# Optimization experiments

Measured on AMD Instinct MI355X. Metric: run time of the kernel, lower is better.

The kernel has to match this reference:

```python
import jax, jax.numpy as jnp
import numpy as np

# LinearAdderV1: out[b,o] = sum_i (input[b,i] + weight[o,i]); out *= bias[o]
# The broadcast-add-then-reduce is mathematically separable:
#   sum_i (x[b,i] + w[o,i]) = sum_i x[b,i] + sum_i w[o,i]
# so we compute it without materializing the (B, O, I) intermediate. Same math,
# identical up to fp summation order.

B = 4096
IN = 4096
OUT = 4096


def setup_inputs() -> dict:
    key = jax.random.key(0)
    k1, k2, k3 = jax.random.split(key, 3)
    inp = jax.random.normal(k1, (B, IN), dtype=jnp.float32)
    # kaiming_uniform-ish scale for weight, uniform bias in [-1/sqrt(fan_in), +)
    bound_w = float(np.sqrt(6.0 / ((1.0 + 5.0) * IN)))  # a=sqrt(5) => gain^2=2/(1+5)
    weight = jax.random.uniform(k2, (OUT, IN), dtype=jnp.float32, minval=-bound_w, maxval=bound_w)
    bound_b = float(1.0 / np.sqrt(IN))
    bias_param = jax.random.uniform(k3, (OUT,), dtype=jnp.float32, minval=-bound_b, maxval=bound_b)
    return {"input": inp, "weight": weight, "bias_param": bias_param}


def reference(input, weight, bias_param):
    # (B, 1) + (1, OUT) -> (B, OUT)
    x_sum = jnp.sum(input, axis=-1, keepdims=True)          # (B, 1)
    w_sum = jnp.sum(weight, axis=-1)                        # (OUT,)
    out = x_sum + w_sum[None, :]                            # (B, OUT)
    out = out * bias_param[None, :]
    return out
```

## Files before the change

kernel.cpp:

```cpp
#include <hip/hip_runtime.h>

#define B_DIM   4096
#define IN_DIM  4096
#define OUT_DIM 4096

typedef float floatx4 __attribute__((ext_vector_type(4)));

__global__ __launch_bounds__(256) void rowsum_kernel(
    const float* __restrict__ input, const float* __restrict__ weight,
    const float* __restrict__ bias, float* __restrict__ ws)
{
    const int wave = threadIdx.x >> 6;
    const int lane = threadIdx.x & 63;
    const int row  = blockIdx.x * 4 + wave;

    const float* src = (row < B_DIM)
        ? input  + (size_t)row * IN_DIM
        : weight + (size_t)(row - B_DIM) * IN_DIM;
    const float4* src4 = (const float4*)src;

    float4 v[16];
    #pragma unroll
    for (int k = 0; k < 16; ++k)
        v[k] = src4[lane + k * 64];

    float s0 = 0.f, s1 = 0.f, s2 = 0.f, s3 = 0.f;
    #pragma unroll
    for (int k = 0; k < 16; k += 4) {
        s0 += (v[k+0].x + v[k+0].y) + (v[k+0].z + v[k+0].w);
        s1 += (v[k+1].x + v[k+1].y) + (v[k+1].z + v[k+1].w);
        s2 += (v[k+2].x + v[k+2].y) + (v[k+2].z + v[k+2].w);
        s3 += (v[k+3].x + v[k+3].y) + (v[k+3].z + v[k+3].w);
    }
    float s = (s0 + s1) + (s2 + s3);

    #pragma unroll
    for (int off = 32; off > 0; off >>= 1)
        s += __shfl_down(s, off, 64);

    if (lane == 0) {
        if (row < B_DIM) {
            ws[row] = s;
        } else {
            const int o = row - B_DIM;
            ws[B_DIM + o] = s * bias[o];
        }
    }
}

__global__ __launch_bounds__(256) void epilogue_kernel(
    const float* __restrict__ bias, const float* __restrict__ ws,
    float* __restrict__ out)
{
    const int b = blockIdx.x;
    const float xs = ws[b];

    const float4* bias4 = (const float4*)bias;
    const float4* wb4   = (const float4*)(ws + B_DIM);
    floatx4* out4 = (floatx4*)out + (size_t)b * (OUT_DIM / 4);

    #pragma unroll
    for (int k = 0; k < 4; ++k) {
        const int i = threadIdx.x + k * 256;
        const float4 bi = bias4[i];
        const float4 w  = wb4[i];
        floatx4 r;
        r.x = fmaf(xs, bi.x, w.x);
        r.y = fmaf(xs, bi.y, w.y);
        r.z = fmaf(xs, bi.z, w.z);
        r.w = fmaf(xs, bi.w, w.w);
        __builtin_nontemporal_store(r, &out4[i]);
    }
}

extern "C" void kernel_launch(void* const* d_in, const int* in_sizes, int n_in,
                              void* d_out, int out_size, void* d_ws, size_t ws_size,
                              hipStream_t stream) {
    const float* input  = (const float*)d_in[0];
    const float* weight = (const float*)d_in[1];
    const float* bias   = (const float*)d_in[2];
    float* out = (float*)d_out;
    float* ws  = (float*)d_ws;

    rowsum_kernel<<<(B_DIM + OUT_DIM) / 4, 256, 0, stream>>>(input, weight, bias, ws);
    epilogue_kernel<<<B_DIM, 256, 0, stream>>>(bias, ws, out);
}
```

Measured before the change: 170.2 us.

## Fuse input row-sum into epilogue kernel and use nontemporal loads

The input row reduction moves out of the first kernel and into the epilogue. Each block now sums its own input row with a wave shuffle plus a shared-memory reduction, then writes the output row. The first kernel only reduces the weight rows. Both kernels now read their inputs with nontemporal loads. This shrinks the first launch and removes a workspace round trip for the input sums, but the second kernel gains a block-wide sync and more serial work per block.

New measurement: 163.6 us (median of 2 runs). 3.9% less time.

```diff
diff --git a/kernel.cpp b/kernel.cpp
--- a/kernel.cpp
+++ b/kernel.cpp
@@ -6,31 +6,27 @@
 
 typedef float floatx4 __attribute__((ext_vector_type(4)));
 
-__global__ __launch_bounds__(256) void rowsum_kernel(
-    const float* __restrict__ input, const float* __restrict__ weight,
-    const float* __restrict__ bias, float* __restrict__ ws)
+__global__ __launch_bounds__(256) void wsum_kernel(
+    const float* __restrict__ weight, const float* __restrict__ bias,
+    float* __restrict__ wb)
 {
     const int wave = threadIdx.x >> 6;
     const int lane = threadIdx.x & 63;
-    const int row  = blockIdx.x * 4 + wave;
+    const int o    = blockIdx.x * 4 + wave;
 
-    const float* src = (row < B_DIM)
-        ? input  + (size_t)row * IN_DIM
-        : weight + (size_t)(row - B_DIM) * IN_DIM;
-    const float4* src4 = (const float4*)src;
-
-    float4 v[16];
-    #pragma unroll
-    for (int k = 0; k < 16; ++k)
-        v[k] = src4[lane + k * 64];
+    const floatx4* src4 = (const floatx4*)(weight + (size_t)o * IN_DIM);
 
     float s0 = 0.f, s1 = 0.f, s2 = 0.f, s3 = 0.f;
     #pragma unroll
     for (int k = 0; k < 16; k += 4) {
-        s0 += (v[k+0].x + v[k+0].y) + (v[k+0].z + v[k+0].w);
-        s1 += (v[k+1].x + v[k+1].y) + (v[k+1].z + v[k+1].w);
-        s2 += (v[k+2].x + v[k+2].y) + (v[k+2].z + v[k+2].w);
-        s3 += (v[k+3].x + v[k+3].y) + (v[k+3].z + v[k+3].w);
+        floatx4 v0 = __builtin_nontemporal_load(&src4[lane + (k + 0) * 64]);
+        floatx4 v1 = __builtin_nontemporal_load(&src4[lane + (k + 1) * 64]);
+        floatx4 v2 = __builtin_nontemporal_load(&src4[lane + (k + 2) * 64]);
+        floatx4 v3 = __builtin_nontemporal_load(&src4[lane + (k + 3) * 64]);
+        s0 += (v0.x + v0.y) + (v0.z + v0.w);
+        s1 += (v1.x + v1.y) + (v1.z + v1.w);
+        s2 += (v2.x + v2.y) + (v2.z + v2.w);
+        s3 += (v3.x + v3.y) + (v3.z + v3.w);
     }
     float s = (s0 + s1) + (s2 + s3);
 
@@ -38,32 +34,47 @@
     for (int off = 32; off > 0; off >>= 1)
         s += __shfl_down(s, off, 64);
 
-    if (lane == 0) {
-        if (row < B_DIM) {
-            ws[row] = s;
-        } else {
-            const int o = row - B_DIM;
-            ws[B_DIM + o] = s * bias[o];
-        }
-    }
+    if (lane == 0)
+        wb[o] = s * bias[o];
 }
 
-__global__ __launch_bounds__(256) void epilogue_kernel(
-    const float* __restrict__ bias, const float* __restrict__ ws,
-    float* __restrict__ out)
+__global__ __launch_bounds__(256) void fused_kernel(
+    const float* __restrict__ input, const float* __restrict__ bias,
+    const float* __restrict__ wb, float* __restrict__ out)
 {
     const int b = blockIdx.x;
-    const float xs = ws[b];
+    const int t = threadIdx.x;
 
-    const float4* bias4 = (const float4*)bias;
-    const float4* wb4   = (const float4*)(ws + B_DIM);
+    const floatx4* in4 = (const floatx4*)(input + (size_t)b * IN_DIM);
+
+    floatx4 v[4];
+    #pragma unroll
+    for (int k = 0; k < 4; ++k)
+        v[k] = __builtin_nontemporal_load(&in4[t + k * 256]);
+
+    float s = 0.f;
+    #pragma unroll
+    for (int k = 0; k < 4; ++k)
+        s += (v[k].x + v[k].y) + (v[k].z + v[k].w);
+
+    #pragma unroll
+    for (int off = 32; off > 0; off >>= 1)
+        s += __shfl_down(s, off, 64);
+
+    __shared__ float sm[4];
+    if ((t & 63) == 0) sm[t >> 6] = s;
+    __syncthreads();
+    const float xs = (sm[0] + sm[1]) + (sm[2] + sm[3]);
+
+    const floatx4* bias4 = (const floatx4*)bias;
+    const floatx4* wb4   = (const floatx4*)wb;
     floatx4* out4 = (floatx4*)out + (size_t)b * (OUT_DIM / 4);
 
     #pragma unroll
     for (int k = 0; k < 4; ++k) {
-        const int i = threadIdx.x + k * 256;
-        const float4 bi = bias4[i];
-        const float4 w  = wb4[i];
+        const int i = t + k * 256;
+        const floatx4 bi = bias4[i];
+        const floatx4 w  = wb4[i];
         floatx4 r;
         r.x = fmaf(xs, bi.x, w.x);
         r.y = fmaf(xs, bi.y, w.y);
@@ -80,8 +91,8 @@
     const float* weight = (const float*)d_in[1];
     const float* bias   = (const float*)d_in[2];
     float* out = (float*)d_out;
-    float* ws  = (float*)d_ws;
+    float* wb  = (float*)d_ws;
 
-    rowsum_kernel<<<(B_DIM + OUT_DIM) / 4, 256, 0, stream>>>(input, weight, bias, ws);
-    epilogue_kernel<<<B_DIM, 256, 0, stream>>>(bias, ws, out);
+    wsum_kernel<<<OUT_DIM / 4, 256, 0, stream>>>(weight, bias, wb);
+    fused_kernel<<<B_DIM, 256, 0, stream>>>(input, bias, wb, out);
 }
```

## Split row reductions into per-wave chunks combined with atomics, add zeroing kernel

Applied to the files above, without the earlier changes.

Each wave now reduces one 256-float chunk of a row across 16 strided slabs, with a one-ahead software prefetch, and accumulates partial sums into the workspace via atomicAdd. A new kernel zeroes the workspace first. The epilogue becomes a flat grid-stride write that computes (xs + wsum) * bias. The goal is more parallelism and better load distribution across the input and weight streams, at the cost of an extra launch, atomics, and a different summation order.

After: 175.1 us. 1.03x slower.

```diff
diff --git a/kernel.cpp b/kernel.cpp
--- a/kernel.cpp
+++ b/kernel.cpp
@@ -6,70 +6,69 @@
 
 typedef float floatx4 __attribute__((ext_vector_type(4)));
 
-__global__ __launch_bounds__(256) void rowsum_kernel(
+
+__global__ __launch_bounds__(256) void k0_zero(float* __restrict__ ws) {
+    ws[blockIdx.x * 256 + threadIdx.x] = 0.f;
+}
+
+__global__ __launch_bounds__(256) void k1_reduce(
     const float* __restrict__ input, const float* __restrict__ weight,
-    const float* __restrict__ bias, float* __restrict__ ws)
+    float* __restrict__ ws)
 {
     const int wave = threadIdx.x >> 6;
     const int lane = threadIdx.x & 63;
-    const int row  = blockIdx.x * 4 + wave;
+    const int w    = blockIdx.x * 4 + wave;
+    const int fi   = w * 64 + lane;
+    const int rowi = w >> 4;
 
-    const float* src = (row < B_DIM)
-        ? input  + (size_t)row * IN_DIM
-        : weight + (size_t)(row - B_DIM) * IN_DIM;
-    const float4* src4 = (const float4*)src;
+    const floatx4* inp4 = (const floatx4*)input;
+    const floatx4* wgt4 = (const floatx4*)weight;
 
-    float4 v[16];
+    floatx4 cur = inp4[fi];
     #pragma unroll
-    for (int k = 0; k < 16; ++k)
-        v[k] = src4[lane + k * 64];
+    for (int k = 0; k < 16; ++k) {
+        floatx4 nxt = cur;
+        if (k < 7)        nxt = inp4[(k + 1) * 524288 + fi];
+        else if (k < 15)  nxt = wgt4[(k - 7) * 524288 + fi];
 
-    float s0 = 0.f, s1 = 0.f, s2 = 0.f, s3 = 0.f;
-    #pragma unroll
-    for (int k = 0; k < 16; k += 4) {
-        s0 += (v[k+0].x + v[k+0].y) + (v[k+0].z + v[k+0].w);
-        s1 += (v[k+1].x + v[k+1].y) + (v[k+1].z + v[k+1].w);
-        s2 += (v[k+2].x + v[k+2].y) + (v[k+2].z + v[k+2].w);
-        s3 += (v[k+3].x + v[k+3].y) + (v[k+3].z + v[k+3].w);
-    }
-    float s = (s0 + s1) + (s2 + s3);
+        float s = (cur.x + cur.y) + (cur.z + cur.w);
+        #pragma unroll
+        for (int off = 32; off > 0; off >>= 1)
+            s += __shfl_down(s, off, 64);
 
-    #pragma unroll
-    for (int off = 32; off > 0; off >>= 1)
-        s += __shfl_down(s, off, 64);
-
-    if (lane == 0) {
-        if (row < B_DIM) {
-            ws[row] = s;
-        } else {
-            const int o = row - B_DIM;
-            ws[B_DIM + o] = s * bias[o];
+        if (lane == 0) {
+            const int slot = (k < 8) ? (k * 512 + rowi)
+                                     : (4096 + (k - 8) * 512 + rowi);
+            atomicAdd(&ws[slot], s);
         }
+        cur = nxt;
     }
 }
 
-__global__ __launch_bounds__(256) void epilogue_kernel(
+__global__ __launch_bounds__(256) void k2_write(
     const float* __restrict__ bias, const float* __restrict__ ws,
     float* __restrict__ out)
 {
-    const int b = blockIdx.x;
-    const float xs = ws[b];
-
-    const float4* bias4 = (const float4*)bias;
-    const float4* wb4   = (const float4*)(ws + B_DIM);
-    floatx4* out4 = (floatx4*)out + (size_t)b * (OUT_DIM / 4);
+    const int g = blockIdx.x * 256 + threadIdx.x;
+    const floatx4* bias4 = (const floatx4*)bias;
+    const floatx4* wsw4  = (const floatx4*)(ws + 4096);
+    floatx4* out4 = (floatx4*)out;
 
     #pragma unroll
-    for (int k = 0; k < 4; ++k) {
-        const int i = threadIdx.x + k * 256;
-        const float4 bi = bias4[i];
-        const float4 w  = wb4[i];
+    for (int i = 0; i < 8; ++i) {
+        const int idx = i * 524288 + g;
+        const int b   = idx >> 10;
+        const int o4  = idx & 1023;
+
+        const float   xs = ws[b];
+        const floatx4 bi = bias4[o4];
+        const floatx4 wv = wsw4[o4];
         floatx4 r;
-        r.x = fmaf(xs, bi.x, w.x);
-        r.y = fmaf(xs, bi.y, w.y);
-        r.z = fmaf(xs, bi.z, w.z);
-        r.w = fmaf(xs, bi.w, w.w);
-        __builtin_nontemporal_store(r, &out4[i]);
+        r.x = (xs + wv.x) * bi.x;
+        r.y = (xs + wv.y) * bi.y;
+        r.z = (xs + wv.z) * bi.z;
+        r.w = (xs + wv.w) * bi.w;
+        __builtin_nontemporal_store(r, &out4[idx]);
     }
 }
 
@@ -82,6 +81,7 @@
     float* out = (float*)d_out;
     float* ws  = (float*)d_ws;
 
-    rowsum_kernel<<<(B_DIM + OUT_DIM) / 4, 256, 0, stream>>>(input, weight, bias, ws);
-    epilogue_kernel<<<B_DIM, 256, 0, stream>>>(bias, ws, out);
+    k0_zero  <<<32,   256, 0, stream>>>(ws);
+    k1_reduce<<<2048, 256, 0, stream>>>(input, weight, ws);
+    k2_write <<<2048, 256, 0, stream>>>(bias, ws, out);
 }
```
